# Optimization experiments

Measured on AMD Instinct MI355X. Metric: run time of the kernel, lower is better.

## Reference

```python
import jax, jax.numpy as jnp
import numpy as np

B, S, D = 8, 1024, 1024
H, KV, HD = 16, 16, 64
NDIM = 2
EPS = 1e-6


def rms_norm(x, weight=None, eps=EPS):
    var = jnp.mean(jnp.square(x), axis=-1, keepdims=True)
    out = x * jax.lax.rsqrt(var + eps)
    if weight is not None:
        out = out * weight
    return out


def rotate_half(x):
    half = x.shape[-1] // 2
    return jnp.concatenate((-x[..., half:], x[..., :half]), axis=-1)


def multidim_rope(x, cos, sin, ndim):
    # x: [B,S,H,HD]; cos,sin: [B,S,HD]; head_dim split into ndim contiguous
    # chunks of size per = 2*(HD // (2*ndim)); rotate-half applied per chunk.
    b, s, h, hd = x.shape
    per = 2 * (hd // (2 * ndim))
    xg = x.reshape(b, s, h, ndim, per)
    cg = cos.reshape(b, s, 1, ndim, per)
    sg = sin.reshape(b, s, 1, ndim, per)
    out = xg * cg + rotate_half(xg) * sg
    return out.reshape(b, s, h, hd)


def setup_inputs() -> dict:
    key = jax.random.key(0)
    ks = jax.random.split(key, 10)
    scale = 1.0 / np.sqrt(D)
    return {
        "hidden_states": jax.random.normal(ks[0], (B, S, D), jnp.float32),
        "cos": jax.random.uniform(ks[1], (B, S, HD), jnp.float32, -1.0, 1.0),
        "sin": jax.random.uniform(ks[2], (B, S, HD), jnp.float32, -1.0, 1.0),
        "position_ids": jax.random.randint(ks[3], (B, S, NDIM), 0, 32, jnp.int32),
        "wq": jax.random.normal(ks[4], (D, H * HD), jnp.float32) * scale,
        "wk": jax.random.normal(ks[5], (D, KV * HD), jnp.float32) * scale,
        "wv": jax.random.normal(ks[6], (D, KV * HD), jnp.float32) * scale,
        "wo": jax.random.normal(ks[7], (H * HD, D), jnp.float32) * scale,
        "q_norm_w": jnp.ones((HD,), jnp.float32),
        "k_norm_w": jnp.ones((HD,), jnp.float32),
    }


def reference(hidden_states, cos, sin, position_ids, wq, wk, wv, wo, q_norm_w, k_norm_w):
    b, s, _ = hidden_states.shape
    ndim = position_ids.shape[-1]

    q = (hidden_states @ wq).reshape(b, s, H, HD)
    q = rms_norm(q, q_norm_w)
    q = multidim_rope(q, cos, sin, ndim)

    k = (hidden_states @ wk).reshape(b, s, KV, HD)
    k = rms_norm(k, k_norm_w)
    k = multidim_rope(k, cos, sin, ndim)

    v = (hidden_states @ wv).reshape(b, s, KV, HD)
    v = rms_norm(v, None)  # v_norm has no weight

    # Full (non-causal) vision attention, scaling = 1.0
    scores = jnp.einsum("bqhd,bkhd->bhqk", q, k)
    probs = jax.nn.softmax(scores, axis=-1)
    attn = jnp.einsum("bhqk,bkhd->bqhd", probs, v).reshape(b, s, H * HD)

    return attn @ wo
```

## Files before the change

kernel.cpp:

```cpp
#include <hip/hip_runtime.h>
#include <hip/hip_bf16.h>

typedef __attribute__((ext_vector_type(8))) short bf16x8;
typedef __attribute__((ext_vector_type(4))) short bf16x4;
typedef __attribute__((ext_vector_type(4))) float f32x4;

struct __align__(16) V16 { unsigned long long a, b; };

__device__ __forceinline__ float bf2f(unsigned short u) {
  union { unsigned int i; float f; } c; c.i = ((unsigned int)u) << 16; return c.f;
}
__device__ __forceinline__ unsigned short f2bf(float f) {
  unsigned int u; __builtin_memcpy(&u, &f, 4);
  u += 0x7FFFu + ((u >> 16) & 1u);
  return (unsigned short)(u >> 16);
}

__device__ __forceinline__ void async16(unsigned short* lds,
                                        const unsigned short* g) {
  __builtin_amdgcn_global_load_lds(
      (const __attribute__((address_space(1))) unsigned int*)g,
      (__attribute__((address_space(3))) unsigned int*)lds, 16, 0, 0);
}

#define FP32_MAGIC 0x3F800000u

__device__ __forceinline__ void cvt_seg(
    const void* __restrict__ src, unsigned short* __restrict__ dst,
    int n4, int i, int stride, bool f32)
{
  if (f32) {
    const float* s = (const float*)src;
    for (; i < n4; i += stride) {
      float4 v = *(const float4*)(s + (size_t)i * 4);
      ushort2 lo = { f2bf(v.x), f2bf(v.y) };
      ushort2 hi = { f2bf(v.z), f2bf(v.w) };
      *(ushort2*)(dst + (size_t)i * 4)     = lo;
      *(ushort2*)(dst + (size_t)i * 4 + 2) = hi;
    }
  } else {
    const unsigned short* s = (const unsigned short*)src;
    for (; i < n4; i += stride)
      *(ushort4*)(dst + (size_t)i * 4) = *(const ushort4*)(s + (size_t)i * 4);
  }
}

__global__ __launch_bounds__(256) void cvt_bf16(
    const void* __restrict__ src, size_t srcOff,
    unsigned short* __restrict__ dst, int n4,
    const unsigned int* __restrict__ fmt)
{
  const bool f32 = (fmt[0] == FP32_MAGIC);
  const int i = blockIdx.x * blockDim.x + threadIdx.x;
  const int stride = gridDim.x * blockDim.x;
  const void* s = f32 ? (const void*)((const float*)src + srcOff)
                      : (const void*)((const unsigned short*)src + srcOff);
  cvt_seg(s, dst, n4, i, stride, f32);
}

__global__ __launch_bounds__(256) void cvt_all(
    const void* __restrict__ hid, const void* __restrict__ cosr,
    const void* __restrict__ sinr, const void* __restrict__ qnw,
    const void* __restrict__ knw,
    unsigned short* __restrict__ hb, unsigned short* __restrict__ csb,
    unsigned short* __restrict__ snb, unsigned short* __restrict__ qnb,
    unsigned short* __restrict__ knb,
    int hidden_n4, const unsigned int* __restrict__ fmt)
{
  const bool f32 = (fmt[0] == FP32_MAGIC);
  const int bx = blockIdx.x, tid = threadIdx.x;
  if (bx < 2048) {
    if (hidden_n4 > 0)
      cvt_seg(hid, hb, hidden_n4, bx * 256 + tid, 2048 * 256, f32);
  } else if (bx < 2176) {
    cvt_seg(cosr, csb, 131072, (bx - 2048) * 256 + tid, 128 * 256, f32);
  } else if (bx < 2304) {
    cvt_seg(sinr, snb, 131072, (bx - 2176) * 256 + tid, 128 * 256, f32);
  } else {
    if (tid < 16)       cvt_seg(qnw, qnb, 16, tid, 16, f32);
    else if (tid < 32)  cvt_seg(knw, knb, 16, tid - 16, 16, f32);
  }
}

__global__ __launch_bounds__(256) void cvt_t4(
    const void* __restrict__ s0, const void* __restrict__ s1,
    const void* __restrict__ s2, const void* __restrict__ s3,
    unsigned short* __restrict__ d0, unsigned short* __restrict__ d1,
    unsigned short* __restrict__ d2, unsigned short* __restrict__ d3,
    const unsigned int* __restrict__ fmt)
{
  __shared__ __align__(16) unsigned short T[64][72];
  const int z = blockIdx.z;
  const void* src = (z == 0) ? s0 : (z == 1) ? s1 : (z == 2) ? s2 : s3;
  unsigned short* dstT = (z == 0) ? d0 : (z == 1) ? d1 : (z == 2) ? d2 : d3;

  const bool f32 = (fmt[0] == FP32_MAGIC);
  const int tid = threadIdx.x;
  const int k0 = blockIdx.x * 64, n0 = blockIdx.y * 64;
  const int rl = tid >> 3, cl = (tid & 7) * 8;

#pragma unroll
  for (int p = 0; p < 2; ++p) {
    int r = rl + p * 32;
    int cs = cl ^ (r & 56);
    if (f32) {
      const float* s = (const float*)src + (size_t)(k0 + r) * 1024 + n0 + cl;
      float4 v0 = *(const float4*)s, v1 = *(const float4*)(s + 4);
      unsigned short* t = &T[r][cs];
      t[0]=f2bf(v0.x); t[1]=f2bf(v0.y); t[2]=f2bf(v0.z); t[3]=f2bf(v0.w);
      t[4]=f2bf(v1.x); t[5]=f2bf(v1.y); t[6]=f2bf(v1.z); t[7]=f2bf(v1.w);
    } else {
      *(V16*)&T[r][cs] = *(const V16*)((const unsigned short*)src +
                                        (size_t)(k0 + r) * 1024 + n0 + cl);
    }
  }
  __syncthreads();

#pragma unroll
  for (int p = 0; p < 2; ++p) {
    int u = tid + p * 256;
    int d = u >> 3, sc = (u & 7) * 8;
    unsigned short tmp[8];
#pragma unroll
    for (int i = 0; i < 8; ++i) tmp[i] = T[sc + i][d ^ sc];
    *(V16*)&dstT[(size_t)(n0 + d) * 1024 + k0 + sc] = *(V16*)tmp;
  }
}

__global__ __launch_bounds__(256) void transpose_v(
    const unsigned short* __restrict__ v, unsigned short* __restrict__ vt)
{
  __shared__ __align__(16) unsigned short T[64][72];
  const int tid = threadIdx.x;
  const int s0 = blockIdx.x * 64;
  const int bh = blockIdx.y;
  const int b = bh >> 4, h = bh & 15;
  const int rl = tid >> 3, cl = (tid & 7) * 8;

#pragma unroll
  for (int p = 0; p < 2; ++p) {
    int r = rl + p * 32;
    *(V16*)&T[r][cl ^ (r & 56)] = *(const V16*)(
        v + (size_t)(b * 1024 + s0 + r) * 1024 + h * 64 + cl);
  }
  __syncthreads();

#pragma unroll
  for (int p = 0; p < 2; ++p) {
    int u = tid + p * 256;
    int d = u >> 3, sc = (u & 7) * 8;
    unsigned short tmp[8];
#pragma unroll
    for (int i = 0; i < 8; ++i) tmp[i] = T[sc + i][d ^ sc];
    *(V16*)&vt[(size_t)(bh * 64 + d) * 1024 + s0 + sc] = *(V16*)tmp;
  }
}

#define TM 128
#define TN 128
#define TK 64
#define GK 1024

__global__ __launch_bounds__(256) void gemm_qkv(
    const unsigned short* __restrict__ A,
    const unsigned short* __restrict__ Bt,
    unsigned short* __restrict__ Cq,
    unsigned short* __restrict__ Ck,
    unsigned short* __restrict__ Cv,
    const unsigned short* __restrict__ cs,
    const unsigned short* __restrict__ sn,
    const unsigned short* __restrict__ qw,
    const unsigned short* __restrict__ kw,
    int M)
{
  __shared__ __align__(16) unsigned short As[2][TM][TK];
  __shared__ __align__(16) unsigned short Bs[2][TN][TK];

  const int tid  = threadIdx.x;
  const int wave = tid >> 6;
  const int lane = tid & 63;
  const int quad = lane >> 4;
  const int l16  = lane & 15;
  const int bm = blockIdx.x * TM;
  const int bn = blockIdx.y * TN;
  const int wm = (wave & 1) * 64;
  const int wn = (wave >> 1) * 64;

  const f32x4 z = {0.f, 0.f, 0.f, 0.f};
  f32x4 acc[4][4];
#pragma unroll
  for (int i = 0; i < 4; ++i)
#pragma unroll
    for (int j = 0; j < 4; ++j) acc[i][j] = z;

  const int lrow = lane >> 3;
  const int gcol = ((lane & 7) ^ lrow) * 8;
  const unsigned short* aP = A  + (size_t)(bm + wave * 8 + lrow) * GK + gcol;
  const unsigned short* bP = Bt + (size_t)(bn + wave * 8 + lrow) * GK + gcol;
  const int cswz = l16 & 7;

  auto STAGE = [&](int buf, int t) {
#pragma unroll
    for (int p = 0; p < 4; ++p) {
      async16(&As[buf][p * 32 + wave * 8][0], aP + t * TK + p * 32 * GK);
      async16(&Bs[buf][p * 32 + wave * 8][0], bP + t * TK + p * 32 * GK);
    }
  };

  STAGE(0, 0);
  __syncthreads();

#pragma unroll 2
  for (int t = 0; t < GK / TK; ++t) {
    const int cur = t & 1;
    if (t < GK / TK - 1) STAGE(cur ^ 1, t + 1);
#pragma unroll
    for (int s = 0; s < 2; ++s) {
      const int pc = ((s * 4 + quad) ^ cswz) * 8;
      bf16x8 af[4], bfv[4];
#pragma unroll
      for (int mt = 0; mt < 4; ++mt)
        af[mt] = *(const bf16x8*)&As[cur][wm + mt * 16 + l16][pc];
#pragma unroll
      for (int nt = 0; nt < 4; ++nt)
        bfv[nt] = *(const bf16x8*)&Bs[cur][wn + nt * 16 + l16][pc];
#pragma unroll
      for (int mt = 0; mt < 4; ++mt)
#pragma unroll
        for (int nt = 0; nt < 4; ++nt)
          acc[mt][nt] = __builtin_amdgcn_mfma_f32_16x16x32_bf16(
              af[mt], bfv[nt], acc[mt][nt], 0, 0, 0);
    }
    __syncthreads();
  }

  const int which = bn >> 10;
  unsigned short* Cd = (which == 0) ? Cq : (which == 1) ? Ck : Cv;
  const int colbase = (bn & 1023) + wn;

  float wgt[4];
#pragma unroll
  for (int nt = 0; nt < 4; ++nt) {
    int d = nt * 16 + l16;
    wgt[nt] = (which == 0) ? bf2f(qw[d]) * 1.44269504f
            : (which == 1) ? bf2f(kw[d]) : 1.f;
  }

#pragma unroll
  for (int mt = 0; mt < 4; ++mt)
#pragma unroll
    for (int r = 0; r < 4; ++r) {
      const int row = bm + wm + mt * 16 + quad * 4 + r;
      float x0 = acc[mt][0][r], x1 = acc[mt][1][r];
      float x2 = acc[mt][2][r], x3 = acc[mt][3][r];
      float ss = x0 * x0 + x1 * x1 + x2 * x2 + x3 * x3;
      ss += __shfl_xor(ss, 1);
      ss += __shfl_xor(ss, 2);
      ss += __shfl_xor(ss, 4);
      ss += __shfl_xor(ss, 8);
      const float inv = rsqrtf(ss * (1.f / 64.f) + 1e-6f);
      float y[4] = { x0 * inv * wgt[0], x1 * inv * wgt[1],
                     x2 * inv * wgt[2], x3 * inv * wgt[3] };
      float outv[4];
      if (which < 2) {
        const unsigned short* cp = cs + (size_t)row * 64 + l16;
        const unsigned short* sp = sn + (size_t)row * 64 + l16;
#pragma unroll
        for (int nt = 0; nt < 4; ++nt) {
          float c = bf2f(cp[nt * 16]), s = bf2f(sp[nt * 16]);
          float part = (nt & 1) ? y[nt ^ 1] : -y[nt ^ 1];
          outv[nt] = y[nt] * c + part * s;
        }
      } else {
#pragma unroll
        for (int nt = 0; nt < 4; ++nt) outv[nt] = y[nt];
      }
#pragma unroll
      for (int nt = 0; nt < 4; ++nt)
        Cd[(size_t)row * 1024 + colbase + nt * 16 + l16] = f2bf(outv[nt]);
    }
}

__global__ __launch_bounds__(256) void gemm_bf16(
    const unsigned short* __restrict__ A,
    const unsigned short* __restrict__ Bt,
    void* __restrict__ C, size_t cOff,
    const unsigned int* __restrict__ outFmt,
    int M, int N)
{
  __shared__ __align__(16) unsigned short As[2][TM][TK];
  __shared__ __align__(16) unsigned short Bs[2][TN][TK];

  const int tid  = threadIdx.x;
  const int wave = tid >> 6;
  const int lane = tid & 63;
  const int quad = lane >> 4;
  const int l16  = lane & 15;
  const int bm = blockIdx.x * TM;
  const int bn = blockIdx.y * TN;
  const int wm = (wave & 1) * 64;
  const int wn = (wave >> 1) * 64;

  const f32x4 z = {0.f, 0.f, 0.f, 0.f};
  f32x4 acc[4][4];
#pragma unroll
  for (int i = 0; i < 4; ++i)
#pragma unroll
    for (int j = 0; j < 4; ++j) acc[i][j] = z;

  const int lrow = lane >> 3;
  const int gcol = ((lane & 7) ^ lrow) * 8;
  const unsigned short* aP = A  + (size_t)(bm + wave * 8 + lrow) * GK + gcol;
  const unsigned short* bP = Bt + (size_t)(bn + wave * 8 + lrow) * GK + gcol;
  const int cswz = l16 & 7;

  auto STAGE = [&](int buf, int t) {
#pragma unroll
    for (int p = 0; p < 4; ++p) {
      async16(&As[buf][p * 32 + wave * 8][0], aP + t * TK + p * 32 * GK);
      async16(&Bs[buf][p * 32 + wave * 8][0], bP + t * TK + p * 32 * GK);
    }
  };

  STAGE(0, 0);
  __syncthreads();

#pragma unroll 2
  for (int t = 0; t < GK / TK; ++t) {
    const int cur = t & 1;
    if (t < GK / TK - 1) STAGE(cur ^ 1, t + 1);
#pragma unroll
    for (int s = 0; s < 2; ++s) {
      const int pc = ((s * 4 + quad) ^ cswz) * 8;
      bf16x8 af[4], bfv[4];
#pragma unroll
      for (int mt = 0; mt < 4; ++mt)
        af[mt] = *(const bf16x8*)&As[cur][wm + mt * 16 + l16][pc];
#pragma unroll
      for (int nt = 0; nt < 4; ++nt)
        bfv[nt] = *(const bf16x8*)&Bs[cur][wn + nt * 16 + l16][pc];
#pragma unroll
      for (int mt = 0; mt < 4; ++mt)
#pragma unroll
        for (int nt = 0; nt < 4; ++nt)
          acc[mt][nt] = __builtin_amdgcn_mfma_f32_16x16x32_bf16(
              af[mt], bfv[nt], acc[mt][nt], 0, 0, 0);
    }
    __syncthreads();
  }

  const bool of32 = (outFmt != nullptr) && (outFmt[0] == FP32_MAGIC);
  float* Cf = (float*)C + cOff;
  unsigned short* Ch = (unsigned short*)C + cOff;

#pragma unroll
  for (int mt = 0; mt < 4; ++mt)
#pragma unroll
    for (int nt = 0; nt < 4; ++nt)
#pragma unroll
      for (int r = 0; r < 4; ++r) {
        int row = bm + wm + mt * 16 + quad * 4 + r;
        int col = bn + wn + nt * 16 + l16;
        size_t idx = (size_t)row * N + col;
        if (of32) Cf[idx] = acc[mt][nt][r];
        else      Ch[idx] = f2bf(acc[mt][nt][r]);
      }
}

__global__ __launch_bounds__(256) void attn_fused(
    const unsigned short* __restrict__ q,
    const unsigned short* __restrict__ k,
    const unsigned short* __restrict__ vt,
    unsigned short* __restrict__ o)
{
  __shared__ __align__(16) unsigned short Ks[2][64][64];
  __shared__ __align__(16) unsigned short Vs[2][64][64];

  const int tid  = threadIdx.x;
  const int wave = tid >> 6;
  const int lane = tid & 63;
  const int quad = lane >> 4;
  const int l16  = lane & 15;
  const int bh = blockIdx.y;
  const int b  = bh >> 4, h = bh & 15;
  const int qbase = blockIdx.x * 64 + wave * 16;
  const size_t bbase = (size_t)b * 1024;

  bf16x8 qf[2];
  {
    const unsigned short* qp = q + (bbase + qbase + l16) * 1024 + h * 64;
    qf[0] = *(const bf16x8*)(qp + quad * 8);
    qf[1] = *(const bf16x8*)(qp + 32 + quad * 8);
  }

  const f32x4 z = {0.f, 0.f, 0.f, 0.f};
  f32x4 of[5];
#pragma unroll
  for (int nt = 0; nt < 5; ++nt) of[nt] = z;
  float m_run = -1e30f;

  const bf16x8 onesv = { 0x3F80, 0x3F80, 0x3F80, 0x3F80,
                         0x3F80, 0x3F80, 0x3F80, 0x3F80 };

  const int lrow = lane >> 3;
  const int gcol = ((lane & 7) ^ lrow) * 8;
  const unsigned short* kP = k  + (bbase + wave * 8 + lrow) * 1024 + h * 64 + gcol;
  const unsigned short* vP = vt + ((size_t)bh * 64 + wave * 8 + lrow) * 1024 + gcol;
  const int cswz = l16 & 7;

  auto STAGE = [&](int buf, int kt) {
#pragma unroll
    for (int p = 0; p < 2; ++p) {
      async16(&Ks[buf][p * 32 + wave * 8][0], kP + ((size_t)kt * 64 + p * 32) * 1024);
      async16(&Vs[buf][p * 32 + wave * 8][0], vP + (size_t)p * 32 * 1024 + kt * 64);
    }
  };

  STAGE(0, 0);
  __syncthreads();

#pragma unroll 2
  for (int kt = 0; kt < 16; ++kt) {
    const int cur = kt & 1;
    if (kt < 15) STAGE(cur ^ 1, kt + 1);

    f32x4 sf[4];
#pragma unroll
    for (int nt = 0; nt < 4; ++nt) sf[nt] = z;
    __builtin_amdgcn_s_setprio(1);
#pragma unroll
    for (int s = 0; s < 2; ++s) {
      const int pc = ((s * 4 + quad) ^ cswz) * 8;
#pragma unroll
      for (int nt = 0; nt < 4; ++nt) {
        bf16x8 kf = *(const bf16x8*)&Ks[cur][nt * 16 + l16][pc];
        sf[nt] = __builtin_amdgcn_mfma_f32_16x16x32_bf16(kf, qf[s], sf[nt], 0, 0, 0);
      }
    }
    __builtin_amdgcn_s_setprio(0);

    float m0 = fmaxf(fmaxf(sf[0][0], sf[0][1]), fmaxf(sf[0][2], sf[0][3]));
    float m1 = fmaxf(fmaxf(sf[1][0], sf[1][1]), fmaxf(sf[1][2], sf[1][3]));
    float m2 = fmaxf(fmaxf(sf[2][0], sf[2][1]), fmaxf(sf[2][2], sf[2][3]));
    float m3 = fmaxf(fmaxf(sf[3][0], sf[3][1]), fmaxf(sf[3][2], sf[3][3]));
    float mx = fmaxf(fmaxf(m0, m1), fmaxf(m2, m3));
    mx = fmaxf(mx, __shfl_xor(mx, 16));
    mx = fmaxf(mx, __shfl_xor(mx, 32));

    if (!__all(mx - m_run <= 11.5f)) {
      float mn = fmaxf(m_run, mx);
      float alpha = __builtin_amdgcn_exp2f(m_run - mn);
      m_run = mn;
      float ar[4];
#pragma unroll
      for (int r = 0; r < 4; ++r) ar[r] = __shfl(alpha, quad * 4 + r);
#pragma unroll
      for (int nt = 0; nt < 5; ++nt)
#pragma unroll
        for (int r = 0; r < 4; ++r) of[nt][r] *= ar[r];
    }

    bf16x8 pf[2];
#pragma unroll
    for (int nt = 0; nt < 4; ++nt)
#pragma unroll
      for (int r = 0; r < 4; ++r)
        pf[nt >> 1][(nt & 1) * 4 + r] =
            (short)f2bf(__builtin_amdgcn_exp2f(sf[nt][r] - m_run));

    __builtin_amdgcn_s_setprio(1);
#pragma unroll
    for (int s = 0; s < 2; ++s) {
#pragma unroll
      for (int nt = 0; nt < 4; ++nt) {
        const unsigned short* vrow = &Vs[cur][nt * 16 + l16][0];
        const int g0  = (4 * s + (quad >> 1)) ^ cswz;
        const int off = 4 * (quad & 1);
        bf16x4 v0 = *(const bf16x4*)(vrow + g0 * 8 + off);
        bf16x4 v1 = *(const bf16x4*)(vrow + (g0 ^ 2) * 8 + off);
        bf16x8 vf = __builtin_shufflevector(v0, v1, 0, 1, 2, 3, 4, 5, 6, 7);
        of[nt] = __builtin_amdgcn_mfma_f32_16x16x32_bf16(pf[s], vf, of[nt], 0, 0, 0);
      }
      of[4] = __builtin_amdgcn_mfma_f32_16x16x32_bf16(pf[s], onesv, of[4], 0, 0, 0);
    }
    __builtin_amdgcn_s_setprio(0);

    __syncthreads();
  }

  float invl[4];
#pragma unroll
  for (int r = 0; r < 4; ++r) invl[r] = 1.f / of[4][r];
#pragma unroll
  for (int nt = 0; nt < 4; ++nt)
#pragma unroll
    for (int r = 0; r < 4; ++r) {
      int row = qbase + quad * 4 + r;
      o[(bbase + row) * 1024 + h * 64 + nt * 16 + l16] = f2bf(of[nt][r] * invl[r]);
    }
}

extern "C" void kernel_launch(void* const* d_in, const int* in_sizes, int n_in,
                              void* d_out, int out_size, void* d_ws, size_t ws_size,
                              hipStream_t stream) {
  const void* hidden = d_in[0];
  const void* cosr   = d_in[1];
  const void* sinr   = d_in[2];
  const void* wq     = d_in[4];
  const void* wk     = d_in[5];
  const void* wv     = d_in[6];
  const void* wo     = d_in[7];
  const void* qnw    = d_in[8];
  const void* knw    = d_in[9];
  const unsigned int* fmt = (const unsigned int*)qnw;

  const size_t MEG = 1024 * 1024;
  dim3 blk(256);
  unsigned short* w = (unsigned short*)d_ws;

  if (ws_size >= (size_t)60 * MEG) {
    unsigned short* hb   = w;
    unsigned short* vtb  = w;
    unsigned short* wqT  = w + 8 * MEG;
    unsigned short* wkT  = w + 9 * MEG;
    unsigned short* wvT  = w + 10 * MEG;
    unsigned short* woT  = w + 11 * MEG;
    unsigned short* csb  = w + 12 * MEG;
    unsigned short* snb  = w + 12 * MEG + 512 * 1024;
    unsigned short* qnb  = w + 13 * MEG;
    unsigned short* knb  = w + 13 * MEG + 64;
    unsigned short* qb   = w + 14 * MEG;
    unsigned short* kb   = w + 22 * MEG;
    unsigned short* vb   = (unsigned short*)d_out;
    unsigned short* ab   = qb;

    cvt_all<<<dim3(2305), blk, 0, stream>>>(hidden, cosr, sinr, qnw, knw,
                                            hb, csb, snb, qnb, knb,
                                            2 * (int)MEG, fmt);
    cvt_t4<<<dim3(16, 16, 4), blk, 0, stream>>>(wq, wk, wv, wo,
                                                wqT, wkT, wvT, woT, fmt);

    const int M = 8192;
    gemm_qkv<<<dim3(M / TM, 24), blk, 0, stream>>>(hb, wqT, qb, kb, vb,
                                                   csb, snb, qnb, knb, M);
    transpose_v<<<dim3(16, 8 * 16), blk, 0, stream>>>(vb, vtb);
    attn_fused<<<dim3(16, 8 * 16), blk, 0, stream>>>(qb, kb, vtb, ab);
    gemm_bf16<<<dim3(M / TM, 8), blk, 0, stream>>>(ab, woT, d_out, 0, fmt,
                                                   M, 1024);
  } else {
    unsigned short* wqT  = w;
    unsigned short* wkT  = w + 1 * MEG;
    unsigned short* wvT  = w + 2 * MEG;
    unsigned short* woT  = w + 3 * MEG;
    unsigned short* csb  = w + 4 * MEG;
    unsigned short* snb  = w + 4 * MEG + 512 * 1024;
    unsigned short* qnb  = w + 5 * MEG;
    unsigned short* knb  = w + 5 * MEG + 64;
    unsigned short* hbb  = w + 6 * MEG;
    unsigned short* qb   = w + 7 * MEG;
    unsigned short* kb   = w + 8 * MEG;
    unsigned short* vb   = w + 9 * MEG;
    unsigned short* vtb  = w + 10 * MEG;

    cvt_t4<<<dim3(16, 16, 4), blk, 0, stream>>>(wq, wk, wv, wo,
                                                wqT, wkT, wvT, woT, fmt);
    cvt_all<<<dim3(2305), blk, 0, stream>>>(hidden, cosr, sinr, qnw, knw,
                                            nullptr, csb, snb, qnb, knb,
                                            0, fmt);

    const int Mb = 1024;
    for (int b = 0; b < 8; ++b) {
      cvt_bf16<<<dim3(512), blk, 0, stream>>>(hidden, (size_t)b * MEG, hbb,
                                              (int)(MEG / 4), fmt);
      gemm_qkv<<<dim3(Mb / TM, 24), blk, 0, stream>>>(
          hbb, wqT, qb, kb, vb, csb + (size_t)b * 64 * 1024,
          snb + (size_t)b * 64 * 1024, qnb, knb, Mb);
      transpose_v<<<dim3(16, 16), blk, 0, stream>>>(vb, vtb);
      attn_fused<<<dim3(16, 16), blk, 0, stream>>>(qb, kb, vtb, qb);
      gemm_bf16<<<dim3(Mb / TM, 8), blk, 0, stream>>>(qb, woT, d_out,
                                                      (size_t)b * MEG, fmt,
                                                      Mb, 1024);
    }
  }
}
```

Before: 286.5 us.

## Single-buffer GEMM LDS tiles and use packed bf16 convert in attention

Both projection GEMMs drop the double-buffered async LDS staging for a single buffer loaded and synchronized each K step. This halves LDS use and may allow more resident blocks, but global loads no longer overlap with MFMA work inside a block. In attention, the softmax probabilities are converted to bf16 with the packed v_cvt_pk_bf16_f32 instruction instead of manual rounding bit math, which cuts VALU instructions in the inner loop.

Result: faster. 279.4 us (-2.5%).

```diff
diff --git a/kernel.cpp b/kernel.cpp
--- a/kernel.cpp
+++ b/kernel.cpp
@@ -173,8 +173,8 @@
     const unsigned short* __restrict__ kw,
     int M)
 {
-  __shared__ __align__(16) unsigned short As[2][TM][TK];
-  __shared__ __align__(16) unsigned short Bs[2][TN][TK];
+  __shared__ __align__(16) unsigned short As[TM][TK];
+  __shared__ __align__(16) unsigned short Bs[TN][TK];
 
   const int tid  = threadIdx.x;
   const int wave = tid >> 6;
@@ -199,31 +199,25 @@
   const unsigned short* bP = Bt + (size_t)(bn + wave * 8 + lrow) * GK + gcol;
   const int cswz = l16 & 7;
 
-  auto STAGE = [&](int buf, int t) {
+  for (int k0 = 0; k0 < GK; k0 += TK) {
 #pragma unroll
     for (int p = 0; p < 4; ++p) {
-      async16(&As[buf][p * 32 + wave * 8][0], aP + t * TK + p * 32 * GK);
-      async16(&Bs[buf][p * 32 + wave * 8][0], bP + t * TK + p * 32 * GK);
-    }
-  };
-
-  STAGE(0, 0);
-  __syncthreads();
-
-#pragma unroll 2
-  for (int t = 0; t < GK / TK; ++t) {
-    const int cur = t & 1;
-    if (t < GK / TK - 1) STAGE(cur ^ 1, t + 1);
+      async16(&As[p * 32 + wave * 8][0], aP + (size_t)p * 32 * GK);
+      async16(&Bs[p * 32 + wave * 8][0], bP + (size_t)p * 32 * GK);
+    }
+    aP += TK; bP += TK;
+    __syncthreads();
+
 #pragma unroll
     for (int s = 0; s < 2; ++s) {
       const int pc = ((s * 4 + quad) ^ cswz) * 8;
       bf16x8 af[4], bfv[4];
 #pragma unroll
       for (int mt = 0; mt < 4; ++mt)
-        af[mt] = *(const bf16x8*)&As[cur][wm + mt * 16 + l16][pc];
+        af[mt] = *(const bf16x8*)&As[wm + mt * 16 + l16][pc];
 #pragma unroll
       for (int nt = 0; nt < 4; ++nt)
-        bfv[nt] = *(const bf16x8*)&Bs[cur][wn + nt * 16 + l16][pc];
+        bfv[nt] = *(const bf16x8*)&Bs[wn + nt * 16 + l16][pc];
 #pragma unroll
       for (int mt = 0; mt < 4; ++mt)
 #pragma unroll
@@ -288,8 +282,8 @@
     const unsigned int* __restrict__ outFmt,
     int M, int N)
 {
-  __shared__ __align__(16) unsigned short As[2][TM][TK];
-  __shared__ __align__(16) unsigned short Bs[2][TN][TK];
+  __shared__ __align__(16) unsigned short As[TM][TK];
+  __shared__ __align__(16) unsigned short Bs[TN][TK];
 
   const int tid  = threadIdx.x;
   const int wave = tid >> 6;
@@ -314,31 +308,25 @@
   const unsigned short* bP = Bt + (size_t)(bn + wave * 8 + lrow) * GK + gcol;
   const int cswz = l16 & 7;
 
-  auto STAGE = [&](int buf, int t) {
+  for (int k0 = 0; k0 < GK; k0 += TK) {
 #pragma unroll
     for (int p = 0; p < 4; ++p) {
-      async16(&As[buf][p * 32 + wave * 8][0], aP + t * TK + p * 32 * GK);
-      async16(&Bs[buf][p * 32 + wave * 8][0], bP + t * TK + p * 32 * GK);
-    }
-  };
-
-  STAGE(0, 0);
-  __syncthreads();
-
-#pragma unroll 2
-  for (int t = 0; t < GK / TK; ++t) {
-    const int cur = t & 1;
-    if (t < GK / TK - 1) STAGE(cur ^ 1, t + 1);
+      async16(&As[p * 32 + wave * 8][0], aP + (size_t)p * 32 * GK);
+      async16(&Bs[p * 32 + wave * 8][0], bP + (size_t)p * 32 * GK);
+    }
+    aP += TK; bP += TK;
+    __syncthreads();
+
 #pragma unroll
     for (int s = 0; s < 2; ++s) {
       const int pc = ((s * 4 + quad) ^ cswz) * 8;
       bf16x8 af[4], bfv[4];
 #pragma unroll
       for (int mt = 0; mt < 4; ++mt)
-        af[mt] = *(const bf16x8*)&As[cur][wm + mt * 16 + l16][pc];
+        af[mt] = *(const bf16x8*)&As[wm + mt * 16 + l16][pc];
 #pragma unroll
       for (int nt = 0; nt < 4; ++nt)
-        bfv[nt] = *(const bf16x8*)&Bs[cur][wn + nt * 16 + l16][pc];
+        bfv[nt] = *(const bf16x8*)&Bs[wn + nt * 16 + l16][pc];
 #pragma unroll
       for (int mt = 0; mt < 4; ++mt)
 #pragma unroll
@@ -460,13 +448,19 @@
         for (int r = 0; r < 4; ++r) of[nt][r] *= ar[r];
     }
 
-    bf16x8 pf[2];
-#pragma unroll
-    for (int nt = 0; nt < 4; ++nt)
-#pragma unroll
-      for (int r = 0; r < 4; ++r)
-        pf[nt >> 1][(nt & 1) * 4 + r] =
-            (short)f2bf(__builtin_amdgcn_exp2f(sf[nt][r] - m_run));
+    union PFU { bf16x8 v; unsigned int w[4]; } pfu[2];
+#pragma unroll
+    for (int nt = 0; nt < 4; ++nt) {
+      float e0 = __builtin_amdgcn_exp2f(sf[nt][0] - m_run);
+      float e1 = __builtin_amdgcn_exp2f(sf[nt][1] - m_run);
+      float e2 = __builtin_amdgcn_exp2f(sf[nt][2] - m_run);
+      float e3 = __builtin_amdgcn_exp2f(sf[nt][3] - m_run);
+      unsigned int w0, w1;
+      asm("v_cvt_pk_bf16_f32 %0, %1, %2" : "=v"(w0) : "v"(e0), "v"(e1));
+      asm("v_cvt_pk_bf16_f32 %0, %1, %2" : "=v"(w1) : "v"(e2), "v"(e3));
+      pfu[nt >> 1].w[(nt & 1) * 2]     = w0;
+      pfu[nt >> 1].w[(nt & 1) * 2 + 1] = w1;
+    }
 
     __builtin_amdgcn_s_setprio(1);
 #pragma unroll
@@ -479,9 +473,9 @@
         bf16x4 v0 = *(const bf16x4*)(vrow + g0 * 8 + off);
         bf16x4 v1 = *(const bf16x4*)(vrow + (g0 ^ 2) * 8 + off);
         bf16x8 vf = __builtin_shufflevector(v0, v1, 0, 1, 2, 3, 4, 5, 6, 7);
-        of[nt] = __builtin_amdgcn_mfma_f32_16x16x32_bf16(pf[s], vf, of[nt], 0, 0, 0);
+        of[nt] = __builtin_amdgcn_mfma_f32_16x16x32_bf16(pfu[s].v, vf, of[nt], 0, 0, 0);
       }
-      of[4] = __builtin_amdgcn_mfma_f32_16x16x32_bf16(pf[s], onesv, of[4], 0, 0, 0);
+      of[4] = __builtin_amdgcn_mfma_f32_16x16x32_bf16(pfu[s].v, onesv, of[4], 0, 0, 0);
     }
     __builtin_amdgcn_s_setprio(0);
 
```
